# Optimization experiments

Hardware: AMD Instinct MI355X
Metric: run time of the kernel (lower is better)

Reference implementation:

```python
import jax, jax.numpy as jnp
import numpy as np

B, R, D, H, L, E, NREL = 8, 1024, 256, 8, 2, 32768, 32
FF = 4 * D
HD = D // H
NEG = -1e9  # finite 'masked' value (stands in for -inf in the sparse attention mask)


def setup_inputs() -> dict:
    key = jax.random.key(0)
    ks = jax.random.split(key, 18)
    s = 0.02
    inp = {
        'node_embeddings': jax.random.normal(ks[0], (B, R, D), jnp.float32),
        'edge_index': jax.random.randint(ks[1], (B, 2, E), 0, R, jnp.int32),
        'relation_id': jax.random.randint(ks[2], (B, E), 0, NREL, jnp.int32),
        'keep_mask': jax.random.randint(ks[3], (B, E), 0, 2, jnp.int32).astype(bool),
        # learned params
        'rel_bias': jax.random.normal(ks[4], (max(NREL, 32), 1), jnp.float32) * s,
        'Wqkv': jax.random.normal(ks[5], (L, 3 * D, D), jnp.float32) * s,
        'bqkv': jnp.zeros((L, 3 * D), jnp.float32),
        'Wo': jax.random.normal(ks[6], (L, D, D), jnp.float32) * s,
        'bo': jnp.zeros((L, D), jnp.float32),
        'ln1_g': jnp.ones((L, D), jnp.float32),
        'ln1_b': jnp.zeros((L, D), jnp.float32),
        'W1': jax.random.normal(ks[7], (L, FF, D), jnp.float32) * s,
        'b1': jnp.zeros((L, FF), jnp.float32),
        'W2': jax.random.normal(ks[8], (L, D, FF), jnp.float32) * s,
        'b2': jnp.zeros((L, D), jnp.float32),
        'ln2_g': jnp.ones((L, D), jnp.float32),
        'ln2_b': jnp.zeros((L, D), jnp.float32),
    }
    return inp


def _layer_norm(x, g, b, eps=1e-5):
    mu = jnp.mean(x, axis=-1, keepdims=True)
    var = jnp.mean(jnp.square(x - mu), axis=-1, keepdims=True)
    return (x - mu) * jax.lax.rsqrt(var + eps) * g + b


def _build_mask(edge_index, relation_id, keep_mask, rel_bias):
    # Vectorized equivalent of the per-batch / per-edge Python loops:
    # base mask: NEG everywhere, 0 at kept edges (and diagonal), then scatter-ADD
    # the per-edge relation bias (duplicate edges accumulate, as in the loop).
    src = edge_index[:, 0, :]  # [B,E]
    dst = edge_index[:, 1, :]  # [B,E]
    bidx = jnp.broadcast_to(jnp.arange(B)[:, None], (B, E))
    mask = jnp.full((B, R, R), NEG, jnp.float32)
    base_vals = jnp.where(keep_mask, 0.0, NEG)
    mask = mask.at[bidx, src, dst].max(base_vals)  # dropped edges leave NEG
    di = jnp.arange(R)
    mask = mask.at[:, di, di].set(0.0)  # self-attention always allowed
    bias = rel_bias[relation_id, 0]  # [B,E]
    mask = mask.at[bidx, src, dst].add(jnp.where(keep_mask, bias, 0.0))
    return mask


def reference(node_embeddings, edge_index, relation_id, keep_mask, rel_bias,
              Wqkv, bqkv, Wo, bo, ln1_g, ln1_b, W1, b1, W2, b2, ln2_g, ln2_b):
    mask = _build_mask(edge_index, relation_id, keep_mask, rel_bias)  # [B,R,R]
    x = node_embeddings
    scale = 1.0 / np.sqrt(HD).astype(np.float32)
    for l in range(L):
        qkv = jnp.einsum('brd,ed->bre', x, Wqkv[l]) + bqkv[l]
        q, k, v = jnp.split(qkv, 3, axis=-1)
        q = q.reshape(B, R, H, HD)
        k = k.reshape(B, R, H, HD)
        v = v.reshape(B, R, H, HD)
        scores = jnp.einsum('bqhd,bkhd->bhqk', q, k) * scale + mask[:, None]
        attn = jax.nn.softmax(scores, axis=-1)
        out = jnp.einsum('bhqk,bkhd->bqhd', attn, v).reshape(B, R, D)
        out = jnp.einsum('brd,ed->bre', out, Wo[l]) + bo[l]
        x = _layer_norm(x + out, ln1_g[l], ln1_b[l])
        h = jax.nn.gelu(jnp.einsum('brd,fd->brf', x, W1[l]) + b1[l], approximate=False)
        h = jnp.einsum('brf,df->brd', h, W2[l]) + b2[l]
        x = _layer_norm(x + h, ln2_g[l], ln2_b[l])
    return x
```

## Files before the change

### kernel.cpp

```cpp
#include <hip/hip_runtime.h>
#include <hip/hip_bf16.h>
#include <math.h>

#define B_ 8
#define R_ 1024
#define D_ 256
#define H_ 8
#define L_ 2
#define E_ 32768
#define FF_ 1024
#define NEGV (-1000000000.0f)

typedef short bf16x8 __attribute__((ext_vector_type(8)));
typedef float f32x4 __attribute__((ext_vector_type(4)));

__device__ __forceinline__ unsigned short f2b(float f){
  unsigned int u = __float_as_uint(f);
  u += 0x7fffu + ((u >> 16) & 1u);
  return (unsigned short)(u >> 16);
}

#define ASYNC_COPY16(gp, lp) \
  __builtin_amdgcn_global_load_lds((const __attribute__((address_space(1))) void*)(gp), \
                                   (__attribute__((address_space(3))) void*)(lp), 16, 0, 0)


__global__ void detect_bool(const unsigned char* __restrict__ km, int* __restrict__ flag){
  int i = blockIdx.x*256 + threadIdx.x;
  int hit = ((i & 3) != 0) && (km[i] != 0);
  if (__ballot(hit) != 0ull && (threadIdx.x & 63) == 0) atomicOr(flag, 1);
}

__global__ void mask_fill(float* __restrict__ mask){
  size_t i = ((size_t)blockIdx.x*256 + threadIdx.x)*4;
  int row = (int)((i >> 10) & 1023);
  int col = (int)(i & 1023);
  float4 v;
  v.x = (row == col+0) ? 0.0f : NEGV;
  v.y = (row == col+1) ? 0.0f : NEGV;
  v.z = (row == col+2) ? 0.0f : NEGV;
  v.w = (row == col+3) ? 0.0f : NEGV;
  *(float4*)&mask[i] = v;
}

__device__ __forceinline__ int keep_of(const unsigned char* km, const int* flag, int tid){
  return flag[0] ? (int)km[tid] : (int)km[(size_t)tid*4];
}

__global__ void edge_base(const int* __restrict__ ei, const unsigned char* __restrict__ km,
                          const int* __restrict__ flag, float* __restrict__ mask){
  int tid = blockIdx.x*256 + threadIdx.x;
  int b = tid >> 15, e = tid & (E_-1);
  if (keep_of(km, flag, tid)){
    int src = ei[(size_t)b*2*E_ + e];
    int dst = ei[(size_t)b*2*E_ + E_ + e];
    mask[((size_t)b*R_ + src)*R_ + dst] = 0.0f;
  }
}

__global__ void edge_bias(const int* __restrict__ ei, const int* __restrict__ rid,
                          const unsigned char* __restrict__ km, const int* __restrict__ flag,
                          const float* __restrict__ rb, float* __restrict__ mask){
  int tid = blockIdx.x*256 + threadIdx.x;
  int b = tid >> 15, e = tid & (E_-1);
  if (keep_of(km, flag, tid)){
    int src = ei[(size_t)b*2*E_ + e];
    int dst = ei[(size_t)b*2*E_ + E_ + e];
    atomicAdd(&mask[((size_t)b*R_ + src)*R_ + dst], rb[rid[tid]]);
  }
}


__global__ void cvt_bf16(const float* __restrict__ src, unsigned short* __restrict__ dst, int n){
  int i = (blockIdx.x*256 + threadIdx.x)*4;
  if (i >= n) return;
  float4 v = *(const float4*)&src[i];
  ushort4 o;
  o.x = f2b(v.x); o.y = f2b(v.y); o.z = f2b(v.z); o.w = f2b(v.w);
  *(ushort4*)&dst[i] = o;
}

template<int MODE>
__global__ __launch_bounds__(256) void gemm_bt(const unsigned short* __restrict__ A,
    const unsigned short* __restrict__ Bw, const float* __restrict__ bias,
    void* __restrict__ Cout, int M, int N, int K)
{
  __shared__ unsigned short As[128*32];
  __shared__ unsigned short Bs[128*32];
  const int nb = N >> 7;
  const int bm = blockIdx.x / nb, bn = blockIdx.x % nb;
  const int m0 = bm << 7, n0 = bn << 7;
  const int t = threadIdx.x, lane = t & 63, wid = t >> 6;
  const int wr = wid >> 1, wc = wid & 1;
  const int c = lane & 15, g = lane >> 4;

  f32x4 zz = {0.f,0.f,0.f,0.f};
  f32x4 acc[4][4];
  #pragma unroll
  for (int mi=0; mi<4; mi++)
    #pragma unroll
    for (int ni=0; ni<4; ni++) acc[mi][ni] = zz;

  for (int k0 = 0; k0 < K; k0 += 32){
    __syncthreads();
    #pragma unroll
    for (int it=0; it<2; ++it){
      int chunk = wid*2 + it;
      int idx = chunk*64 + lane;
      int row = idx >> 2, seg = idx & 3;
      ASYNC_COPY16(A  + (size_t)(m0+row)*K + k0 + seg*8, &As[chunk*512]);
      ASYNC_COPY16(Bw + (size_t)(n0+row)*K + k0 + seg*8, &Bs[chunk*512]);
    }
    __syncthreads();
    bf16x8 af[4], bfr[4];
    #pragma unroll
    for (int mi=0; mi<4; mi++) af[mi]  = *(const bf16x8*)&As[(wr*64 + mi*16 + c)*32 + g*8];
    #pragma unroll
    for (int ni=0; ni<4; ni++) bfr[ni] = *(const bf16x8*)&Bs[(wc*64 + ni*16 + c)*32 + g*8];
    #pragma unroll
    for (int mi=0; mi<4; mi++)
      #pragma unroll
      for (int ni=0; ni<4; ni++)
        acc[mi][ni] = __builtin_amdgcn_mfma_f32_16x16x32_bf16(af[mi], bfr[ni], acc[mi][ni], 0,0,0);
  }

  #pragma unroll
  for (int mi=0; mi<4; mi++){
    #pragma unroll
    for (int ni=0; ni<4; ni++){
      int col = n0 + wc*64 + ni*16 + c;
      float bv = bias[col];
      #pragma unroll
      for (int r=0; r<4; r++){
        int row = m0 + wr*64 + mi*16 + 4*g + r;
        float v = acc[mi][ni][r] + bv;
        if (MODE == 2) v = 0.5f*v*(1.0f + erff(v*0.70710678f));
        if (MODE == 1) ((float*)Cout)[(size_t)row*N + col] = v;
        else           ((unsigned short*)Cout)[(size_t)row*N + col] = f2b(v);
      }
    }
  }
}

__global__ __launch_bounds__(256) void attn_kernel(const unsigned short* __restrict__ qkv,
    const float* __restrict__ mask, unsigned short* __restrict__ aout)
{
  __shared__ unsigned short Klds[128*40];
  __shared__ unsigned short VT[32*136];
  __shared__ unsigned short P[4*32*136];
  const int blk = blockIdx.x;
  const int qt = blk & 7, h = (blk >> 3) & 7, b = blk >> 6;
  const int t = threadIdx.x, lane = t & 63, wid = t >> 6;
  const int c = lane & 15, g = lane >> 4;
  const int q0 = qt*128;
  const size_t qbase = (size_t)b*R_*768;
  const float scale = 0.17677669529663689f;

  bf16x8 qf[2];
  #pragma unroll
  for (int fr=0; fr<2; ++fr){
    int qr = q0 + wid*32 + fr*16 + c;
    qf[fr] = *(const bf16x8*)&qkv[qbase + (size_t)qr*768 + h*32 + g*8];
  }

  f32x4 z4 = {0.f,0.f,0.f,0.f};
  f32x4 oacc[2][2];
  float mrun[2][4], lrun[2][4];
  #pragma unroll
  for (int fr=0; fr<2; ++fr){
    oacc[fr][0] = z4; oacc[fr][1] = z4;
    #pragma unroll
    for (int r=0; r<4; r++){ mrun[fr][r] = -1e30f; lrun[fr][r] = 0.f; }
  }
  unsigned short* Pw = &P[wid*32*136];

  for (int kt=0; kt<8; ++kt){
    const int kv0 = kt*128;
    __syncthreads();
    #pragma unroll
    for (int it=0; it<2; ++it){
      int idx = it*256 + t, row = idx >> 2, seg = idx & 3;
      uint4 kd = *(const uint4*)&qkv[qbase + (size_t)(kv0+row)*768 + 256 + h*32 + seg*8];
      *(uint4*)&Klds[row*40 + seg*8] = kd;
    }
    {
      int d = t & 31, rb8 = t >> 5;
      __align__(16) unsigned short tv[16];
      #pragma unroll
      for (int j=0; j<16; j++)
        tv[j] = qkv[qbase + (size_t)(kv0 + rb8*16 + j)*768 + 512 + h*32 + d];
      *(uint4*)&VT[d*136 + rb8*16]     = *(const uint4*)&tv[0];
      *(uint4*)&VT[d*136 + rb8*16 + 8] = *(const uint4*)&tv[8];
    }
    __syncthreads();

    f32x4 sacc[2][8];
    #pragma unroll
    for (int fc=0; fc<8; ++fc){
      bf16x8 kb = *(const bf16x8*)&Klds[(fc*16 + c)*40 + g*8];
      sacc[0][fc] = __builtin_amdgcn_mfma_f32_16x16x32_bf16(qf[0], kb, z4, 0,0,0);
      sacc[1][fc] = __builtin_amdgcn_mfma_f32_16x16x32_bf16(qf[1], kb, z4, 0,0,0);
    }
    #pragma unroll
    for (int fr=0; fr<2; ++fr)
      #pragma unroll
      for (int fc=0; fc<8; ++fc)
        #pragma unroll
        for (int r=0; r<4; r++){
          int qr = q0 + wid*32 + fr*16 + 4*g + r;
          float mv = mask[((size_t)b*R_ + qr)*R_ + kv0 + fc*16 + c];
          sacc[fr][fc][r] = sacc[fr][fc][r]*scale + mv;
        }
    #pragma unroll
    for (int fr=0; fr<2; ++fr)
      #pragma unroll
      for (int r=0; r<4; r++){
        float mx = sacc[fr][0][r];
        #pragma unroll
        for (int fc=1; fc<8; ++fc) mx = fmaxf(mx, sacc[fr][fc][r]);
        mx = fmaxf(mx, __shfl_xor(mx, 1));
        mx = fmaxf(mx, __shfl_xor(mx, 2));
        mx = fmaxf(mx, __shfl_xor(mx, 4));
        mx = fmaxf(mx, __shfl_xor(mx, 8));
        float mnew  = fmaxf(mrun[fr][r], mx);
        float alpha = __expf(mrun[fr][r] - mnew);
        float sum = 0.f;
        #pragma unroll
        for (int fc=0; fc<8; ++fc){
          float pv = __expf(sacc[fr][fc][r] - mnew);
          sacc[fr][fc][r] = pv;
          sum += pv;
        }
        sum += __shfl_xor(sum, 1); sum += __shfl_xor(sum, 2);
        sum += __shfl_xor(sum, 4); sum += __shfl_xor(sum, 8);
        lrun[fr][r] = lrun[fr][r]*alpha + sum;
        mrun[fr][r] = mnew;
        oacc[fr][0][r] *= alpha;
        oacc[fr][1][r] *= alpha;
      }
    #pragma unroll
    for (int fr=0; fr<2; ++fr)
      #pragma unroll
      for (int fc=0; fc<8; ++fc)
        #pragma unroll
        for (int r=0; r<4; r++)
          Pw[(fr*16 + 4*g + r)*136 + fc*16 + c] = f2b(sacc[fr][fc][r]);
    #pragma unroll
    for (int ks=0; ks<4; ++ks){
      bf16x8 pa0 = *(const bf16x8*)&Pw[(c)*136      + ks*32 + g*8];
      bf16x8 pa1 = *(const bf16x8*)&Pw[(16 + c)*136 + ks*32 + g*8];
      #pragma unroll
      for (int dg=0; dg<2; ++dg){
        bf16x8 vb = *(const bf16x8*)&VT[(dg*16 + c)*136 + ks*32 + g*8];
        oacc[0][dg] = __builtin_amdgcn_mfma_f32_16x16x32_bf16(pa0, vb, oacc[0][dg], 0,0,0);
        oacc[1][dg] = __builtin_amdgcn_mfma_f32_16x16x32_bf16(pa1, vb, oacc[1][dg], 0,0,0);
      }
    }
  }
  #pragma unroll
  for (int fr=0; fr<2; ++fr)
    #pragma unroll
    for (int dg=0; dg<2; ++dg)
      #pragma unroll
      for (int r=0; r<4; r++){
        int qr = q0 + wid*32 + fr*16 + 4*g + r;
        float o = oacc[fr][dg][r] / lrun[fr][r];
        aout[((size_t)b*R_ + qr)*D_ + h*32 + dg*16 + c] = f2b(o);
      }
}

__global__ __launch_bounds__(256) void resid_ln(const float* __restrict__ xin,
    const float* __restrict__ res, const float* __restrict__ gg, const float* __restrict__ bb,
    float* __restrict__ xout, unsigned short* __restrict__ xbf)
{
  int row = blockIdx.x*4 + (threadIdx.x >> 6);
  int lane = threadIdx.x & 63;
  size_t base = (size_t)row*D_ + lane*4;
  float4 a  = *(const float4*)&xin[base];
  float4 rr = *(const float4*)&res[base];
  float y0 = a.x+rr.x, y1 = a.y+rr.y, y2 = a.z+rr.z, y3 = a.w+rr.w;
  float s = y0+y1+y2+y3;
  #pragma unroll
  for (int off=32; off>=1; off>>=1) s += __shfl_xor(s, off);
  float mu = s * (1.0f/256.0f);
  float d0=y0-mu, d1=y1-mu, d2=y2-mu, d3=y3-mu;
  float q = d0*d0 + d1*d1 + d2*d2 + d3*d3;
  #pragma unroll
  for (int off=32; off>=1; off>>=1) q += __shfl_xor(q, off);
  float rstd = rsqrtf(q*(1.0f/256.0f) + 1e-5f);
  float4 gv = *(const float4*)&gg[lane*4];
  float4 bv = *(const float4*)&bb[lane*4];
  float o0 = d0*rstd*gv.x + bv.x;
  float o1 = d1*rstd*gv.y + bv.y;
  float o2 = d2*rstd*gv.z + bv.z;
  float o3 = d3*rstd*gv.w + bv.w;
  float4 o; o.x=o0; o.y=o1; o.z=o2; o.w=o3;
  *(float4*)&xout[base] = o;
  ushort4 ob; ob.x=f2b(o0); ob.y=f2b(o1); ob.z=f2b(o2); ob.w=f2b(o3);
  *(ushort4*)&xbf[base] = ob;
}

extern "C" void kernel_launch(void* const* d_in, const int* in_sizes, int n_in,
                              void* d_out, int out_size, void* d_ws, size_t ws_size,
                              hipStream_t stream)
{
  const float* node = (const float*)d_in[0];
  const int*   ei   = (const int*)d_in[1];
  const int*   rid  = (const int*)d_in[2];
  const unsigned char* km = (const unsigned char*)d_in[3];
  const float* rb   = (const float*)d_in[4];
  const float* Wqkv = (const float*)d_in[5];
  const float* bqkv = (const float*)d_in[6];
  const float* Wo   = (const float*)d_in[7];
  const float* bo   = (const float*)d_in[8];
  const float* ln1g = (const float*)d_in[9];
  const float* ln1b = (const float*)d_in[10];
  const float* W1   = (const float*)d_in[11];
  const float* b1   = (const float*)d_in[12];
  const float* W2   = (const float*)d_in[13];
  const float* b2   = (const float*)d_in[14];
  const float* ln2g = (const float*)d_in[15];
  const float* ln2b = (const float*)d_in[16];

  char* ws = (char*)d_ws;
  int*   flag = (int*)ws;
  float* mask = (float*)(ws + 256);
  unsigned short* wqkv_b = (unsigned short*)(ws + 33554688);
  unsigned short* wo_b   = (unsigned short*)(ws + 34341120);
  unsigned short* w1_b   = (unsigned short*)(ws + 34603264);
  unsigned short* w2_b   = (unsigned short*)(ws + 35651840);
  unsigned short* x_bf   = (unsigned short*)(ws + 36700416);
  unsigned short* qkvb   = (unsigned short*)(ws + 40894720);
  unsigned short* ao     = (unsigned short*)(ws + 53477632);
  float* xf   = (float*)(ws + 57671936);
  float* tmp  = (float*)(ws + 66060544);
  unsigned short* hbuf   = (unsigned short*)(ws + 74449152);

  hipMemsetAsync(flag, 0, 4, stream);
  detect_bool<<<1024, 256, 0, stream>>>(km, flag);
  mask_fill<<<8192, 256, 0, stream>>>(mask);
  edge_base<<<1024, 256, 0, stream>>>(ei, km, flag, mask);
  edge_bias<<<1024, 256, 0, stream>>>(ei, rid, km, flag, rb, mask);

  cvt_bf16<<<384, 256, 0, stream>>>(Wqkv, wqkv_b, L_*768*256);
  cvt_bf16<<<128, 256, 0, stream>>>(Wo,   wo_b,   L_*256*256);
  cvt_bf16<<<512, 256, 0, stream>>>(W1,   w1_b,   L_*1024*256);
  cvt_bf16<<<512, 256, 0, stream>>>(W2,   w2_b,   L_*256*1024);
  cvt_bf16<<<2048,256, 0, stream>>>(node, x_bf,   B_*R_*D_);

  for (int l = 0; l < L_; ++l){
    gemm_bt<0><<<384, 256, 0, stream>>>(x_bf, wqkv_b + l*196608, bqkv + l*768, qkvb, 8192, 768, 256);
    attn_kernel<<<512, 256, 0, stream>>>(qkvb, mask, ao);
    gemm_bt<1><<<128, 256, 0, stream>>>(ao, wo_b + l*65536, bo + l*256, tmp, 8192, 256, 256);
    resid_ln<<<2048, 256, 0, stream>>>(l==0 ? node : xf, tmp, ln1g + l*256, ln1b + l*256, xf, x_bf);
    gemm_bt<2><<<512, 256, 0, stream>>>(x_bf, w1_b + l*262144, b1 + l*1024, hbuf, 8192, 1024, 256);
    gemm_bt<1><<<128, 256, 0, stream>>>(hbuf, w2_b + l*262144, b2 + l*256, tmp, 8192, 256, 1024);
    float* outp = (l == L_-1) ? (float*)d_out : xf;
    resid_ln<<<2048, 256, 0, stream>>>(xf, tmp, ln2g + l*256, ln2b + l*256, outp, x_bf);
  }
}
```

Baseline: 369.0 us.

## Restructure attention to transposed MFMA with register P and narrower N=256 GEMM tiles

The attention kernel now computes S^T (K as the A operand), so each lane owns one query row. This allows vectorized float4 mask loads, only cross-lane shuffles of 16/32 for the softmax reductions, and register-resident P passed to the PV MFMA through shuffles instead of an LDS round-trip. Blocks grow to 512 threads with 16 query rows per wave. The N=256 GEMMs (Wo and W2) switch to a 128x64 tile to double the block count and improve CU fill. The trade-offs are extra shuffle instructions and lower per-block reuse in the GEMMs.

```diff
diff --git a/kernel.cpp b/kernel.cpp
--- a/kernel.cpp
+++ b/kernel.cpp
@@ -18,6 +18,12 @@
   unsigned int u = __float_as_uint(f);
   u += 0x7fffu + ((u >> 16) & 1u);
   return (unsigned short)(u >> 16);
+}
+
+__device__ __forceinline__ unsigned int pk_bf16(float lo, float hi){
+  unsigned int r;
+  asm volatile("v_cvt_pk_bf16_f32 %0, %1, %2" : "=v"(r) : "v"(lo), "v"(hi));
+  return r;
 }
 
 #define ASYNC_COPY16(gp, lp) \
@@ -80,55 +86,63 @@
   *(ushort4*)&dst[i] = o;
 }
 
-template<int MODE>
+template<int MODE, int BN>
 __global__ __launch_bounds__(256) void gemm_bt(const unsigned short* __restrict__ A,
     const unsigned short* __restrict__ Bw, const float* __restrict__ bias,
     void* __restrict__ Cout, int M, int N, int K)
 {
+  constexpr int NI = BN/32;
+  constexpr int NCH = 8 + BN/16;
+  constexpr int CPW = NCH/4;
   __shared__ unsigned short As[128*32];
-  __shared__ unsigned short Bs[128*32];
-  const int nb = N >> 7;
+  __shared__ unsigned short Bs[BN*32];
+  const int nb = N / BN;
   const int bm = blockIdx.x / nb, bn = blockIdx.x % nb;
-  const int m0 = bm << 7, n0 = bn << 7;
+  const int m0 = bm << 7, n0 = bn * BN;
   const int t = threadIdx.x, lane = t & 63, wid = t >> 6;
   const int wr = wid >> 1, wc = wid & 1;
   const int c = lane & 15, g = lane >> 4;
 
   f32x4 zz = {0.f,0.f,0.f,0.f};
-  f32x4 acc[4][4];
+  f32x4 acc[4][NI];
   #pragma unroll
   for (int mi=0; mi<4; mi++)
     #pragma unroll
-    for (int ni=0; ni<4; ni++) acc[mi][ni] = zz;
+    for (int ni=0; ni<NI; ni++) acc[mi][ni] = zz;
 
   for (int k0 = 0; k0 < K; k0 += 32){
     __syncthreads();
     #pragma unroll
-    for (int it=0; it<2; ++it){
-      int chunk = wid*2 + it;
-      int idx = chunk*64 + lane;
-      int row = idx >> 2, seg = idx & 3;
-      ASYNC_COPY16(A  + (size_t)(m0+row)*K + k0 + seg*8, &As[chunk*512]);
-      ASYNC_COPY16(Bw + (size_t)(n0+row)*K + k0 + seg*8, &Bs[chunk*512]);
+    for (int it=0; it<CPW; ++it){
+      int chunk = wid*CPW + it;
+      int row16 = lane >> 2, seg = lane & 3;
+      if (chunk < 8){
+        int row = chunk*16 + row16;
+        ASYNC_COPY16(A + (size_t)(m0+row)*K + k0 + seg*8, &As[chunk*512]);
+      } else {
+        int bch = chunk - 8;
+        int row = bch*16 + row16;
+        ASYNC_COPY16(Bw + (size_t)(n0+row)*K + k0 + seg*8, &Bs[bch*512]);
+      }
     }
     __syncthreads();
-    bf16x8 af[4], bfr[4];
+    bf16x8 af[4], bfr[NI];
     #pragma unroll
     for (int mi=0; mi<4; mi++) af[mi]  = *(const bf16x8*)&As[(wr*64 + mi*16 + c)*32 + g*8];
     #pragma unroll
-    for (int ni=0; ni<4; ni++) bfr[ni] = *(const bf16x8*)&Bs[(wc*64 + ni*16 + c)*32 + g*8];
+    for (int ni=0; ni<NI; ni++) bfr[ni] = *(const bf16x8*)&Bs[(wc*(BN/2) + ni*16 + c)*32 + g*8];
     #pragma unroll
     for (int mi=0; mi<4; mi++)
       #pragma unroll
-      for (int ni=0; ni<4; ni++)
+      for (int ni=0; ni<NI; ni++)
         acc[mi][ni] = __builtin_amdgcn_mfma_f32_16x16x32_bf16(af[mi], bfr[ni], acc[mi][ni], 0,0,0);
   }
 
   #pragma unroll
   for (int mi=0; mi<4; mi++){
     #pragma unroll
-    for (int ni=0; ni<4; ni++){
-      int col = n0 + wc*64 + ni*16 + c;
+    for (int ni=0; ni<NI; ni++){
+      int col = n0 + wc*(BN/2) + ni*16 + c;
       float bv = bias[col];
       #pragma unroll
       for (int r=0; r<4; r++){
@@ -142,131 +156,123 @@
   }
 }
 
-__global__ __launch_bounds__(256) void attn_kernel(const unsigned short* __restrict__ qkv,
+__global__ __launch_bounds__(512, 4) void attn_kernel(const unsigned short* __restrict__ qkv,
     const float* __restrict__ mask, unsigned short* __restrict__ aout)
 {
   __shared__ unsigned short Klds[128*40];
   __shared__ unsigned short VT[32*136];
-  __shared__ unsigned short P[4*32*136];
   const int blk = blockIdx.x;
   const int qt = blk & 7, h = (blk >> 3) & 7, b = blk >> 6;
-  const int t = threadIdx.x, lane = t & 63, wid = t >> 6;
+  const int t = threadIdx.x, lane = t & 63, w = t >> 6;
   const int c = lane & 15, g = lane >> 4;
-  const int q0 = qt*128;
+  const int qrow = qt*128 + w*16 + c;
   const size_t qbase = (size_t)b*R_*768;
   const float scale = 0.17677669529663689f;
 
-  bf16x8 qf[2];
-  #pragma unroll
-  for (int fr=0; fr<2; ++fr){
-    int qr = q0 + wid*32 + fr*16 + c;
-    qf[fr] = *(const bf16x8*)&qkv[qbase + (size_t)qr*768 + h*32 + g*8];
-  }
+  bf16x8 qf = *(const bf16x8*)&qkv[qbase + (size_t)qrow*768 + h*32 + g*8];
 
   f32x4 z4 = {0.f,0.f,0.f,0.f};
-  f32x4 oacc[2][2];
-  float mrun[2][4], lrun[2][4];
-  #pragma unroll
-  for (int fr=0; fr<2; ++fr){
-    oacc[fr][0] = z4; oacc[fr][1] = z4;
-    #pragma unroll
-    for (int r=0; r<4; r++){ mrun[fr][r] = -1e30f; lrun[fr][r] = 0.f; }
-  }
-  unsigned short* Pw = &P[wid*32*136];
+  f32x4 oacc[2] = {z4, z4};
+  float mrun = -1e30f, lrun = 0.f;
+
+  const int srcA = c + ((lane & 16) << 1);
+  const int srcB = srcA + 16;
+  const bool hig = (lane >= 32);
 
   for (int kt=0; kt<8; ++kt){
     const int kv0 = kt*128;
     __syncthreads();
-    #pragma unroll
-    for (int it=0; it<2; ++it){
-      int idx = it*256 + t, row = idx >> 2, seg = idx & 3;
+    {
+      int row = t >> 2, seg = t & 3;
       uint4 kd = *(const uint4*)&qkv[qbase + (size_t)(kv0+row)*768 + 256 + h*32 + seg*8];
       *(uint4*)&Klds[row*40 + seg*8] = kd;
     }
     {
-      int d = t & 31, rb8 = t >> 5;
-      __align__(16) unsigned short tv[16];
-      #pragma unroll
-      for (int j=0; j<16; j++)
-        tv[j] = qkv[qbase + (size_t)(kv0 + rb8*16 + j)*768 + 512 + h*32 + d];
-      *(uint4*)&VT[d*136 + rb8*16]     = *(const uint4*)&tv[0];
-      *(uint4*)&VT[d*136 + rb8*16 + 8] = *(const uint4*)&tv[8];
+      int d = t & 31, grp = t >> 5;
+      __align__(16) unsigned short tv[8];
+      #pragma unroll
+      for (int j=0; j<8; j++)
+        tv[j] = qkv[qbase + (size_t)(kv0 + grp*8 + j)*768 + 512 + h*32 + d];
+      *(uint4*)&VT[d*136 + grp*8] = *(const uint4*)&tv[0];
     }
     __syncthreads();
 
-    f32x4 sacc[2][8];
+    f32x4 st[8];
     #pragma unroll
     for (int fc=0; fc<8; ++fc){
       bf16x8 kb = *(const bf16x8*)&Klds[(fc*16 + c)*40 + g*8];
-      sacc[0][fc] = __builtin_amdgcn_mfma_f32_16x16x32_bf16(qf[0], kb, z4, 0,0,0);
-      sacc[1][fc] = __builtin_amdgcn_mfma_f32_16x16x32_bf16(qf[1], kb, z4, 0,0,0);
-    }
-    #pragma unroll
-    for (int fr=0; fr<2; ++fr)
-      #pragma unroll
-      for (int fc=0; fc<8; ++fc)
-        #pragma unroll
-        for (int r=0; r<4; r++){
-          int qr = q0 + wid*32 + fr*16 + 4*g + r;
-          float mv = mask[((size_t)b*R_ + qr)*R_ + kv0 + fc*16 + c];
-          sacc[fr][fc][r] = sacc[fr][fc][r]*scale + mv;
-        }
-    #pragma unroll
-    for (int fr=0; fr<2; ++fr)
+      st[fc] = __builtin_amdgcn_mfma_f32_16x16x32_bf16(kb, qf, z4, 0,0,0);
+    }
+    const float* mrow = &mask[((size_t)b*R_ + qrow)*R_ + kv0];
+    #pragma unroll
+    for (int fc=0; fc<8; ++fc){
+      float4 mv = *(const float4*)&mrow[fc*16 + 4*g];
+      st[fc][0] = st[fc][0]*scale + mv.x;
+      st[fc][1] = st[fc][1]*scale + mv.y;
+      st[fc][2] = st[fc][2]*scale + mv.z;
+      st[fc][3] = st[fc][3]*scale + mv.w;
+    }
+    float mx = st[0][0];
+    #pragma unroll
+    for (int fc=0; fc<8; ++fc)
+      #pragma unroll
+      for (int r=0; r<4; r++) mx = fmaxf(mx, st[fc][r]);
+    mx = fmaxf(mx, __shfl_xor(mx, 16));
+    mx = fmaxf(mx, __shfl_xor(mx, 32));
+    float mnew  = fmaxf(mrun, mx);
+    float alpha = __expf(mrun - mnew);
+    float sum = 0.f;
+    #pragma unroll
+    for (int fc=0; fc<8; ++fc)
       #pragma unroll
       for (int r=0; r<4; r++){
-        float mx = sacc[fr][0][r];
-        #pragma unroll
-        for (int fc=1; fc<8; ++fc) mx = fmaxf(mx, sacc[fr][fc][r]);
-        mx = fmaxf(mx, __shfl_xor(mx, 1));
-        mx = fmaxf(mx, __shfl_xor(mx, 2));
-        mx = fmaxf(mx, __shfl_xor(mx, 4));
-        mx = fmaxf(mx, __shfl_xor(mx, 8));
-        float mnew  = fmaxf(mrun[fr][r], mx);
-        float alpha = __expf(mrun[fr][r] - mnew);
-        float sum = 0.f;
-        #pragma unroll
-        for (int fc=0; fc<8; ++fc){
-          float pv = __expf(sacc[fr][fc][r] - mnew);
-          sacc[fr][fc][r] = pv;
-          sum += pv;
-        }
-        sum += __shfl_xor(sum, 1); sum += __shfl_xor(sum, 2);
-        sum += __shfl_xor(sum, 4); sum += __shfl_xor(sum, 8);
-        lrun[fr][r] = lrun[fr][r]*alpha + sum;
-        mrun[fr][r] = mnew;
-        oacc[fr][0][r] *= alpha;
-        oacc[fr][1][r] *= alpha;
+        float pv = __expf(st[fc][r] - mnew);
+        st[fc][r] = pv;
+        sum += pv;
       }
-    #pragma unroll
-    for (int fr=0; fr<2; ++fr)
-      #pragma unroll
-      for (int fc=0; fc<8; ++fc)
-        #pragma unroll
-        for (int r=0; r<4; r++)
-          Pw[(fr*16 + 4*g + r)*136 + fc*16 + c] = f2b(sacc[fr][fc][r]);
+    sum += __shfl_xor(sum, 16);
+    sum += __shfl_xor(sum, 32);
+    lrun = lrun*alpha + sum;
+    mrun = mnew;
+    oacc[0][0]*=alpha; oacc[0][1]*=alpha; oacc[0][2]*=alpha; oacc[0][3]*=alpha;
+    oacc[1][0]*=alpha; oacc[1][1]*=alpha; oacc[1][2]*=alpha; oacc[1][3]*=alpha;
+
+    unsigned int u0[8], u1[8];
+    #pragma unroll
+    for (int fc=0; fc<8; ++fc){
+      u0[fc] = pk_bf16(st[fc][0], st[fc][1]);
+      u1[fc] = pk_bf16(st[fc][2], st[fc][3]);
+    }
+
     #pragma unroll
     for (int ks=0; ks<4; ++ks){
-      bf16x8 pa0 = *(const bf16x8*)&Pw[(c)*136      + ks*32 + g*8];
-      bf16x8 pa1 = *(const bf16x8*)&Pw[(16 + c)*136 + ks*32 + g*8];
+      unsigned int e0 = u0[2*ks],   e1 = u1[2*ks];
+      unsigned int o0 = u0[2*ks+1], o1 = u1[2*ks+1];
+      unsigned int w0e = __shfl((int)e0, srcA), w1e = __shfl((int)e1, srcA);
+      unsigned int w2e = __shfl((int)e0, srcB), w3e = __shfl((int)e1, srcB);
+      unsigned int w0o = __shfl((int)o0, srcA), w1o = __shfl((int)o1, srcA);
+      unsigned int w2o = __shfl((int)o0, srcB), w3o = __shfl((int)o1, srcB);
+      union { unsigned int u[4]; bf16x8 v; } pa;
+      pa.u[0] = hig ? w0o : w0e;
+      pa.u[1] = hig ? w1o : w1e;
+      pa.u[2] = hig ? w2o : w2e;
+      pa.u[3] = hig ? w3o : w3e;
       #pragma unroll
       for (int dg=0; dg<2; ++dg){
         bf16x8 vb = *(const bf16x8*)&VT[(dg*16 + c)*136 + ks*32 + g*8];
-        oacc[0][dg] = __builtin_amdgcn_mfma_f32_16x16x32_bf16(pa0, vb, oacc[0][dg], 0,0,0);
-        oacc[1][dg] = __builtin_amdgcn_mfma_f32_16x16x32_bf16(pa1, vb, oacc[1][dg], 0,0,0);
+        oacc[dg] = __builtin_amdgcn_mfma_f32_16x16x32_bf16(vb, pa.v, oacc[dg], 0,0,0);
       }
     }
   }
-  #pragma unroll
-  for (int fr=0; fr<2; ++fr)
-    #pragma unroll
-    for (int dg=0; dg<2; ++dg)
-      #pragma unroll
-      for (int r=0; r<4; r++){
-        int qr = q0 + wid*32 + fr*16 + 4*g + r;
-        float o = oacc[fr][dg][r] / lrun[fr][r];
-        aout[((size_t)b*R_ + qr)*D_ + h*32 + dg*16 + c] = f2b(o);
-      }
+  float rl = 1.0f / lrun;
+  #pragma unroll
+  for (int dg=0; dg<2; ++dg){
+    unsigned int p0 = pk_bf16(oacc[dg][0]*rl, oacc[dg][1]*rl);
+    unsigned int p1 = pk_bf16(oacc[dg][2]*rl, oacc[dg][3]*rl);
+    size_t base = ((size_t)b*R_ + qrow)*D_ + h*32 + dg*16 + 4*g;
+    uint2 pp; pp.x = p0; pp.y = p1;
+    *(uint2*)&aout[base] = pp;
+  }
 }
 
 __global__ __launch_bounds__(256) void resid_ln(const float* __restrict__ xin,
@@ -349,12 +355,12 @@
   cvt_bf16<<<2048,256, 0, stream>>>(node, x_bf,   B_*R_*D_);
 
   for (int l = 0; l < L_; ++l){
-    gemm_bt<0><<<384, 256, 0, stream>>>(x_bf, wqkv_b + l*196608, bqkv + l*768, qkvb, 8192, 768, 256);
-    attn_kernel<<<512, 256, 0, stream>>>(qkvb, mask, ao);
-    gemm_bt<1><<<128, 256, 0, stream>>>(ao, wo_b + l*65536, bo + l*256, tmp, 8192, 256, 256);
+    gemm_bt<0,128><<<384, 256, 0, stream>>>(x_bf, wqkv_b + l*196608, bqkv + l*768, qkvb, 8192, 768, 256);
+    attn_kernel<<<512, 512, 0, stream>>>(qkvb, mask, ao);
+    gemm_bt<1,64><<<256, 256, 0, stream>>>(ao, wo_b + l*65536, bo + l*256, tmp, 8192, 256, 256);
     resid_ln<<<2048, 256, 0, stream>>>(l==0 ? node : xf, tmp, ln1g + l*256, ln1b + l*256, xf, x_bf);
-    gemm_bt<2><<<512, 256, 0, stream>>>(x_bf, w1_b + l*262144, b1 + l*1024, hbuf, 8192, 1024, 256);
-    gemm_bt<1><<<128, 256, 0, stream>>>(hbuf, w2_b + l*262144, b2 + l*256, tmp, 8192, 256, 1024);
+    gemm_bt<2,128><<<512, 256, 0, stream>>>(x_bf, w1_b + l*262144, b1 + l*1024, hbuf, 8192, 1024, 256);
+    gemm_bt<1,64><<<256, 256, 0, stream>>>(hbuf, w2_b + l*262144, b2 + l*256, tmp, 8192, 256, 1024);
     float* outp = (l == L_-1) ? (float*)d_out : xf;
     resid_ln<<<2048, 256, 0, stream>>>(xf, tmp, ln2g + l*256, ln2b + l*256, outp, x_bf);
   }
```

New measurement: 341.7 us. 7.4% less time.
